# Optimization experiments

Hardware: AMD Instinct MI355X
Metric: run time of the kernel (lower is better)

The kernel has to match this reference:

```python
import jax, jax.numpy as jnp
import numpy as np

LAYERS, BLOCKS = 10, 4
NL = LAYERS * BLOCKS
RC, DC, SC, OUT_C = 32, 32, 256, 256
B, T = 4, 32768


def setup_inputs() -> dict:
    key = jax.random.key(0)
    ks = jax.random.split(key, 6)
    s = 0.1  # keep tanh out of saturation
    return {
        "x": jax.random.normal(ks[0], (B, 1, T), jnp.float32),
        "W_start": jax.random.normal(ks[1], (RC, 1), jnp.float32) * s,
        "b_start": jnp.zeros((RC,), jnp.float32),
        "Wd": jax.random.normal(ks[2], (NL, DC, RC, 2), jnp.float32) * s,  # torch conv1d weight (out,in,k)
        "bd": jnp.zeros((NL, DC), jnp.float32),
        "Wr": jax.random.normal(ks[3], (NL, RC, DC), jnp.float32) * s,     # 1x1 residual convs
        "br": jnp.zeros((NL, RC), jnp.float32),
        "Ws": jax.random.normal(ks[4], (NL, SC, DC), jnp.float32) * s,     # 1x1 skip convs
        "bs": jnp.zeros((NL, SC), jnp.float32),
        "Wf": jax.random.normal(ks[5], (OUT_C, SC), jnp.float32) * s,      # final 1x1 conv
        "bf": jnp.zeros((OUT_C,), jnp.float32),
    }


def _forward(x, W_start, b_start, Wd, bd, Wr, br, Ws, bs, Wf, bf):
    # start 1x1 conv: [B,1,T] -> [B,RC,T]
    h = jnp.einsum('oi,bit->bot', W_start, x) + b_start[:, None]
    skip = jnp.zeros((x.shape[0], SC, x.shape[2]), x.dtype)
    for i in range(NL):  # fixed small layer loop (40)
        d = 2 ** (i % LAYERS)
        # causal dilated conv, kernel=2: out[t] = W[...,0]@x[t-d] + W[...,1]@x[t]
        h_shift = jnp.pad(h, ((0, 0), (0, 0), (d, 0)))[:, :, : h.shape[2]]
        z = (jnp.einsum('oi,bit->bot', Wd[i, :, :, 1], h)
             + jnp.einsum('oi,bit->bot', Wd[i, :, :, 0], h_shift)
             + bd[i][:, None])
        z = jnp.tanh(z)
        r = jnp.einsum('oi,bit->bot', Wr[i], z) + br[i][:, None]
        h = h + r  # residual connection
        skip = skip + jnp.einsum('oi,bit->bot', Ws[i], h) + bs[i][:, None]
    out = jax.nn.relu(skip)
    return jnp.einsum('oi,bit->bot', Wf, out) + bf[:, None]


def reference(x, W_start, b_start, Wd, bd, Wr, br, Ws, bs, Wf, bf):
    return _forward(x, W_start, b_start, Wd, bd, Wr, br, Ws, bs, Wf, bf)
```

## Files before the change

### kernel.cpp

```cpp
#include <hip/hip_runtime.h>
#include <hip/hip_bf16.h>

#define T_LEN 32768
#define B_N   4
#define RC    32
#define DC    32
#define SC    256
#define OUTC  256
#define NL    40
#define KTOT  (NL * RC)
#define NBT   (B_N * T_LEN)
#define SLOTB ((size_t)NBT * 32 * 2)
#define BTW   64

typedef float f32x4 __attribute__((ext_vector_type(4)));
typedef short bf16x8 __attribute__((ext_vector_type(8)));
typedef __attribute__((address_space(3))) unsigned int lds_u32;
typedef __attribute__((address_space(3))) char lds_char;
typedef __attribute__((address_space(1))) unsigned int glb_u32;

__device__ __forceinline__ unsigned short f2bf_bits(float f) {
    __hip_bfloat16 b = __float2bfloat16(f);
    unsigned short u;
    __builtin_memcpy(&u, &b, 2);
    return u;
}
__device__ __forceinline__ unsigned pack2(float a, float b) {
    return (unsigned)f2bf_bits(a) | ((unsigned)f2bf_bits(b) << 16);
}
__device__ __forceinline__ float bflo(unsigned u) { return __uint_as_float((u & 0xFFFFu) << 16); }
__device__ __forceinline__ float bfhi(unsigned u) { return __uint_as_float(u & 0xFFFF0000u); }
__device__ __forceinline__ float ftanh(float x) {
    float e = __expf(2.f * x);
    return 1.f - 2.f / (e + 1.f);
}
__device__ __forceinline__ void wait_vmcnt(int n) {
    switch (n) {
        case 0: asm volatile("s_waitcnt vmcnt(0)" ::: "memory"); break;
        case 1: asm volatile("s_waitcnt vmcnt(1)" ::: "memory"); break;
        case 2: asm volatile("s_waitcnt vmcnt(2)" ::: "memory"); break;
        case 4: asm volatile("s_waitcnt vmcnt(4)" ::: "memory"); break;
        default: asm volatile("s_waitcnt vmcnt(8)" ::: "memory"); break;
    }
}

__global__ __launch_bounds__(256) void k_prep(const float* __restrict__ Ws,
                                              const float* __restrict__ Wf,
                                              const float* __restrict__ Wd,
                                              const float* __restrict__ Wr,
                                              const float* __restrict__ bs,
                                              unsigned short* __restrict__ Wsk2,
                                              unsigned short* __restrict__ Wfk,
                                              unsigned short* __restrict__ Wd1k,
                                              unsigned short* __restrict__ Wd0k,
                                              unsigned short* __restrict__ Wrk,
                                              float* __restrict__ bs_sum) {
    int g = blockIdx.x * 256 + threadIdx.x;
    if (g < SC * KTOT) {
        int i = g >> 13, r = g & 8191;
        int oc = r >> 5, c = r & 31;
        Wsk2[g] = f2bf_bits(Ws[(i * SC + oc) * RC + c]);
        return;
    }
    g -= SC * KTOT;
    if (g < OUTC * SC) { Wfk[g] = f2bf_bits(Wf[g]); return; }
    g -= OUTC * SC;
    if (g < NL * 1024) {
        int i = g >> 10, r = g & 1023;
        int o = r >> 5, c = r & 31;
        Wd1k[g] = f2bf_bits(Wd[((i * DC + o) * RC + c) * 2 + 1]);
        return;
    }
    g -= NL * 1024;
    if (g < NL * 1024) {
        int i = g >> 10, r = g & 1023;
        int o = r >> 5, c = r & 31;
        Wd0k[g] = f2bf_bits(Wd[((i * DC + o) * RC + c) * 2 + 0]);
        return;
    }
    g -= NL * 1024;
    if (g < NL * 1024) { Wrk[g] = f2bf_bits(Wr[g]); return; }
    g -= NL * 1024;
    if (g < SC) {
        float s = 0.f;
        for (int i = 0; i < NL; ++i) s += bs[i * SC + g];
        bs_sum[g] = s;
    }
}

__global__ __launch_bounds__(256) void k_start(const float* __restrict__ x,
                                               const float* __restrict__ Wst,
                                               const float* __restrict__ bst,
                                               unsigned short* __restrict__ h0) {
    int g = blockIdx.x * 256 + threadIdx.x;
    float xv = x[g];
    unsigned u[16];
#pragma unroll
    for (int q = 0; q < 16; ++q) {
        float a = Wst[2 * q] * xv + bst[2 * q];
        float b = Wst[2 * q + 1] * xv + bst[2 * q + 1];
        u[q] = pack2(a, b);
    }
    unsigned short* op = h0 + (size_t)g * 32;
#pragma unroll
    for (int q = 0; q < 4; ++q) *(uint4*)&op[q * 8] = *(uint4*)&u[q * 4];
}

__global__ __launch_bounds__(256, 4) void k_layer(const unsigned short* __restrict__ hprev,
                                                  unsigned short* __restrict__ hnext,
                                                  const unsigned short* __restrict__ Wd1k,
                                                  const unsigned short* __restrict__ Wd0k,
                                                  const unsigned short* __restrict__ Wrk,
                                                  const float* __restrict__ bd,
                                                  const float* __restrict__ br,
                                                  int d) {
    __shared__ unsigned short zbuf[4][32 * 40];
    int lane = threadIdx.x & 63;
    int wq = threadIdx.x >> 6;
    int lr = lane & 15, lg = lane >> 4;
    int btb = blockIdx.x * 128 + wq * 32;
    unsigned short* zp = &zbuf[wq][0];

    bf16x8 wd1[2], wd0[2], wr[2];
#pragma unroll
    for (int m = 0; m < 2; ++m) {
        int ao = (m * 16 + lr) * 32 + 8 * lg;
        wd1[m] = *(const bf16x8*)(Wd1k + ao);
        wd0[m] = *(const bf16x8*)(Wd0k + ao);
        wr[m]  = *(const bf16x8*)(Wrk + ao);
    }

    bf16x8 hc[2], hs[2];
    uint2 hcc[2][2];
#pragma unroll
    for (int n = 0; n < 2; ++n) {
        int bt = btb + n * 16 + lr;
        int t = bt & (T_LEN - 1);
        const unsigned short* hp = hprev + (size_t)bt * 32;
        hc[n] = *(const bf16x8*)(hp + 8 * lg);
        int bts = (t >= d) ? (bt - d) : bt;
        bf16x8 v = *(const bf16x8*)(hprev + (size_t)bts * 32 + 8 * lg);
        if (t < d) v = (bf16x8){0, 0, 0, 0, 0, 0, 0, 0};
        hs[n] = v;
#pragma unroll
        for (int m = 0; m < 2; ++m) hcc[n][m] = *(const uint2*)(hp + m * 16 + 4 * lg);
    }

    f32x4 zac[2][2];
#pragma unroll
    for (int m = 0; m < 2; ++m)
#pragma unroll
        for (int n = 0; n < 2; ++n) {
            f32x4 a = __builtin_amdgcn_mfma_f32_16x16x32_bf16(wd0[m], hs[n], (f32x4){0.f, 0.f, 0.f, 0.f}, 0, 0, 0);
            zac[m][n] = __builtin_amdgcn_mfma_f32_16x16x32_bf16(wd1[m], hc[n], a, 0, 0, 0);
        }

#pragma unroll
    for (int m = 0; m < 2; ++m) {
        float4 bdv = *(const float4*)(bd + m * 16 + 4 * lg);
#pragma unroll
        for (int n = 0; n < 2; ++n) {
            int rbt = n * 16 + lr;
            float z0 = ftanh(zac[m][n][0] + bdv.x);
            float z1 = ftanh(zac[m][n][1] + bdv.y);
            float z2 = ftanh(zac[m][n][2] + bdv.z);
            float z3 = ftanh(zac[m][n][3] + bdv.w);
            uint2 u;
            u.x = pack2(z0, z1);
            u.y = pack2(z2, z3);
            *(uint2*)(zp + rbt * 40 + m * 16 + 4 * lg) = u;
        }
    }

    f32x4 racc[2][2];
#pragma unroll
    for (int n = 0; n < 2; ++n) {
        int rbt = n * 16 + lr;
        bf16x8 zb = *(const bf16x8*)(zp + rbt * 40 + 8 * lg);
#pragma unroll
        for (int m = 0; m < 2; ++m)
            racc[m][n] = __builtin_amdgcn_mfma_f32_16x16x32_bf16(wr[m], zb, (f32x4){0.f, 0.f, 0.f, 0.f}, 0, 0, 0);
    }

#pragma unroll
    for (int m = 0; m < 2; ++m) {
        float4 brv = *(const float4*)(br + m * 16 + 4 * lg);
#pragma unroll
        for (int n = 0; n < 2; ++n) {
            int bt = btb + n * 16 + lr;
            float h0 = bflo(hcc[n][m].x) + racc[m][n][0] + brv.x;
            float h1 = bfhi(hcc[n][m].x) + racc[m][n][1] + brv.y;
            float h2 = bflo(hcc[n][m].y) + racc[m][n][2] + brv.z;
            float h3 = bfhi(hcc[n][m].y) + racc[m][n][3] + brv.w;
            uint2 u;
            u.x = pack2(h0, h1);
            u.y = pack2(h2, h3);
            *(uint2*)(hnext + (size_t)bt * 32 + m * 16 + 4 * lg) = u;
        }
    }
}

__global__ __launch_bounds__(512, 2) void k_skipfinal(const unsigned short* __restrict__ hist,
                                                      const unsigned short* __restrict__ Wsk2,
                                                      const unsigned short* __restrict__ Wfk,
                                                      const float* __restrict__ bs_sum,
                                                      const float* __restrict__ bfv,
                                                      float* __restrict__ outp) {
    __shared__ char smem[3 * 20480];
    const int tid = threadIdx.x;
    const int lane = tid & 63, wq = tid >> 6;
    const int lr = lane & 15, lg = lane >> 4;
    const int wm = wq & 3, wn = wq >> 2;
    const int bt0 = blockIdx.x * BTW;
    const char* histb = (const char*)hist;
    const char* Wsb = (const char*)Wsk2;
    lds_char* smem3 = (lds_char*)smem;

    int aoff[4], boff = 0;
    if (wq < 4) {
#pragma unroll
        for (int p = 0; p < 4; ++p) {
            int L = p * 4096 + tid * 16;
            int row = L >> 6, col = L & 63;
            aoff[p] = row * 64 + (col ^ ((row & 3) << 4));
        }
    } else {
        int L = (tid - 256) * 16;
        int row = L >> 6, col = L & 63;
        boff = (bt0 + row) * 64 + (col ^ ((row & 3) << 4));
    }

    auto stage = [&](int k) {
        char* base = smem + (k % 3) * 20480;
        if (wq < 4) {
#pragma unroll
            for (int p = 0; p < 4; ++p)
                __builtin_amdgcn_global_load_lds((const glb_u32*)(Wsb + (size_t)k * 16384 + aoff[p]),
                                                 (lds_u32*)(base + p * 4096 + tid * 16), 16, 0, 0);
        } else {
            __builtin_amdgcn_global_load_lds((const glb_u32*)(histb + (size_t)k * SLOTB + boff),
                                             (lds_u32*)(base + 16384 + (tid - 256) * 16), 16, 0, 0);
        }
    };

    f32x4 acc[4][2];
#pragma unroll
    for (int m = 0; m < 4; ++m)
#pragma unroll
        for (int n = 0; n < 2; ++n) acc[m][n] = (f32x4){0.f, 0.f, 0.f, 0.f};

    const int cswz = (lg * 16) ^ ((lr & 3) << 4);
    const int arow = wm * 64 + lr;
    const int brow = wn * 32 + lr;

    stage(0);
    stage(1);

#pragma unroll
    for (int i = 0; i < NL; ++i) {
        if (i + 2 < NL) stage(i + 2);
        if (wq < 4) wait_vmcnt(i <= 37 ? 8 : (i == 38 ? 4 : 0));
        else        wait_vmcnt(i <= 37 ? 2 : (i == 38 ? 1 : 0));
        __builtin_amdgcn_s_barrier();

        lds_char* Ab = smem3 + (i % 3) * 20480;
        lds_char* Bb = Ab + 16384;
        bf16x8 af0, af1, af2, af3, bf0, bf1;
        asm volatile("ds_read_b128 %0, %1" : "=v"(af0) : "v"(Ab + (arow + 0) * 64 + cswz));
        asm volatile("ds_read_b128 %0, %1" : "=v"(af1) : "v"(Ab + (arow + 16) * 64 + cswz));
        asm volatile("ds_read_b128 %0, %1" : "=v"(af2) : "v"(Ab + (arow + 32) * 64 + cswz));
        asm volatile("ds_read_b128 %0, %1" : "=v"(af3) : "v"(Ab + (arow + 48) * 64 + cswz));
        asm volatile("ds_read_b128 %0, %1" : "=v"(bf0) : "v"(Bb + (brow + 0) * 64 + cswz));
        asm volatile("ds_read_b128 %0, %1" : "=v"(bf1) : "v"(Bb + (brow + 16) * 64 + cswz));
        asm volatile("s_waitcnt lgkmcnt(0)" ::: "memory");
        __builtin_amdgcn_sched_barrier(0);

        acc[0][0] = __builtin_amdgcn_mfma_f32_16x16x32_bf16(af0, bf0, acc[0][0], 0, 0, 0);
        acc[1][0] = __builtin_amdgcn_mfma_f32_16x16x32_bf16(af1, bf0, acc[1][0], 0, 0, 0);
        acc[2][0] = __builtin_amdgcn_mfma_f32_16x16x32_bf16(af2, bf0, acc[2][0], 0, 0, 0);
        acc[3][0] = __builtin_amdgcn_mfma_f32_16x16x32_bf16(af3, bf0, acc[3][0], 0, 0, 0);
        acc[0][1] = __builtin_amdgcn_mfma_f32_16x16x32_bf16(af0, bf1, acc[0][1], 0, 0, 0);
        acc[1][1] = __builtin_amdgcn_mfma_f32_16x16x32_bf16(af1, bf1, acc[1][1], 0, 0, 0);
        acc[2][1] = __builtin_amdgcn_mfma_f32_16x16x32_bf16(af2, bf1, acc[2][1], 0, 0, 0);
        acc[3][1] = __builtin_amdgcn_mfma_f32_16x16x32_bf16(af3, bf1, acc[3][1], 0, 0, 0);
        __builtin_amdgcn_s_barrier();
    }
    __syncthreads();

    char* skb = smem;
#pragma unroll
    for (int m = 0; m < 4; ++m) {
        int oc0 = wm * 64 + m * 16 + lg * 4;
        float c0 = bs_sum[oc0], c1 = bs_sum[oc0 + 1], c2 = bs_sum[oc0 + 2], c3 = bs_sum[oc0 + 3];
#pragma unroll
        for (int n = 0; n < 2; ++n) {
            int bt = wn * 32 + n * 16 + lr;
            f32x4 v = acc[m][n];
            uint2 u;
            u.x = pack2(fmaxf(v[0] + c0, 0.f), fmaxf(v[1] + c1, 0.f));
            u.y = pack2(fmaxf(v[2] + c2, 0.f), fmaxf(v[3] + c3, 0.f));
            int L = bt * 512 + oc0 * 2;
            *(uint2*)(skb + (L ^ ((bt & 7) << 4))) = u;
        }
    }
    __syncthreads();

    f32x4 acc2[4][2];
#pragma unroll
    for (int m = 0; m < 4; ++m)
#pragma unroll
        for (int n = 0; n < 2; ++n) acc2[m][n] = (f32x4){0.f, 0.f, 0.f, 0.f};

    const unsigned short* Fb = Wfk + (size_t)(wm * 64 + lr) * SC + 8 * lg;

#pragma unroll
    for (int kk = 0; kk < SC / 32; ++kk) {
        bf16x8 fa[4];
#pragma unroll
        for (int m = 0; m < 4; ++m) fa[m] = *(const bf16x8*)(Fb + (size_t)m * 16 * SC + kk * 32);
        bf16x8 sbv[2];
#pragma unroll
        for (int n = 0; n < 2; ++n) {
            int bt = wn * 32 + n * 16 + lr;
            int L = bt * 512 + kk * 64 + lg * 16;
            sbv[n] = *(const bf16x8*)(skb + (L ^ ((bt & 7) << 4)));
        }
#pragma unroll
        for (int m = 0; m < 4; ++m)
#pragma unroll
            for (int n = 0; n < 2; ++n)
                acc2[m][n] = __builtin_amdgcn_mfma_f32_16x16x32_bf16(fa[m], sbv[n], acc2[m][n], 0, 0, 0);
    }

    int b2 = bt0 >> 15;
    int t0 = bt0 & (T_LEN - 1);
#pragma unroll
    for (int m = 0; m < 4; ++m) {
        int o0 = wm * 64 + m * 16 + lg * 4;
        float q0 = bfv[o0], q1 = bfv[o0 + 1], q2 = bfv[o0 + 2], q3 = bfv[o0 + 3];
#pragma unroll
        for (int n = 0; n < 2; ++n) {
            int t = t0 + wn * 32 + n * 16 + lr;
            f32x4 v = acc2[m][n];
            outp[((size_t)(b2 * OUTC + o0 + 0) << 15) + t] = v[0] + q0;
            outp[((size_t)(b2 * OUTC + o0 + 1) << 15) + t] = v[1] + q1;
            outp[((size_t)(b2 * OUTC + o0 + 2) << 15) + t] = v[2] + q2;
            outp[((size_t)(b2 * OUTC + o0 + 3) << 15) + t] = v[3] + q3;
        }
    }
}

extern "C" void kernel_launch(void* const* d_in, const int* in_sizes, int n_in,
                              void* d_out, int out_size, void* d_ws, size_t ws_size,
                              hipStream_t stream) {
    const float* x       = (const float*)d_in[0];
    const float* W_start = (const float*)d_in[1];
    const float* b_start = (const float*)d_in[2];
    const float* Wd      = (const float*)d_in[3];
    const float* bd      = (const float*)d_in[4];
    const float* Wr      = (const float*)d_in[5];
    const float* br      = (const float*)d_in[6];
    const float* Ws      = (const float*)d_in[7];
    const float* bs      = (const float*)d_in[8];
    const float* Wf      = (const float*)d_in[9];
    const float* bfv     = (const float*)d_in[10];

    char* wsb = (char*)d_ws;
    unsigned short* Wsk2 = (unsigned short*)(wsb);
    unsigned short* Wfk  = (unsigned short*)(wsb + 655360);
    unsigned short* Wd1k = (unsigned short*)(wsb + 786432);
    unsigned short* Wd0k = (unsigned short*)(wsb + 868352);
    unsigned short* Wrk  = (unsigned short*)(wsb + 950272);
    float*          bs_sum = (float*)(wsb + 1032192);
    char* S1 = wsb + (1 << 20);
    char* X  = S1 + 40 * SLOTB;

    auto slotptr = [&](int i) -> unsigned short* {
        return (unsigned short*)(i == 0 ? X : S1 + (size_t)(i - 1) * SLOTB);
    };

    k_prep<<<(SC * KTOT + OUTC * SC + 3 * NL * 1024 + SC + 255) / 256, 256, 0, stream>>>(
        Ws, Wf, Wd, Wr, bs, Wsk2, Wfk, Wd1k, Wd0k, Wrk, bs_sum);
    k_start<<<NBT / 256, 256, 0, stream>>>(x, W_start, b_start, slotptr(0));

    for (int i = 0; i < NL; ++i) {
        int d = 1 << (i % 10);
        k_layer<<<NBT / 128, 256, 0, stream>>>(slotptr(i), slotptr(i + 1),
                                               Wd1k + i * 1024, Wd0k + i * 1024, Wrk + i * 1024,
                                               bd + i * DC, br + i * RC, d);
    }

    k_skipfinal<<<NBT / BTW, 512, 0, stream>>>((unsigned short*)S1, Wsk2, Wfk, bs_sum, bfv, (float*)d_out);
}
```

Measured before the change: 489.5 us.

## Double skip-GEMM column tile and switch to a two-slot LDS ring

The skip/final kernel now covers 128 time steps per block instead of 64. Each wave computes a 64x64 tile, so every staged slice of skip weights is reused across twice as many columns. Staging moves from a three-slot ring, with waves split between weight and history loads, to a two-slot ring in which every thread loads both. The row swizzle is adjusted to the new tile shapes. The launch-bounds occupancy hint goes from 2 to 4 blocks while accumulators double, which risks register spills. The 64 KB LDS per block may also cap real occupancy below that hint.

```diff
diff --git a/kernel.cpp b/kernel.cpp
--- a/kernel.cpp
+++ b/kernel.cpp
@@ -11,7 +11,8 @@
 #define KTOT  (NL * RC)
 #define NBT   (B_N * T_LEN)
 #define SLOTB ((size_t)NBT * 32 * 2)
-#define BTW   64
+#define BTW   128
+#define RING  24576
 
 typedef float f32x4 __attribute__((ext_vector_type(4)));
 typedef short bf16x8 __attribute__((ext_vector_type(8)));
@@ -34,15 +35,7 @@
     float e = __expf(2.f * x);
     return 1.f - 2.f / (e + 1.f);
 }
-__device__ __forceinline__ void wait_vmcnt(int n) {
-    switch (n) {
-        case 0: asm volatile("s_waitcnt vmcnt(0)" ::: "memory"); break;
-        case 1: asm volatile("s_waitcnt vmcnt(1)" ::: "memory"); break;
-        case 2: asm volatile("s_waitcnt vmcnt(2)" ::: "memory"); break;
-        case 4: asm volatile("s_waitcnt vmcnt(4)" ::: "memory"); break;
-        default: asm volatile("s_waitcnt vmcnt(8)" ::: "memory"); break;
-    }
-}
+__device__ __forceinline__ int swz(int L) { return L ^ ((((L >> 7) & 3)) << 4); }
 
 __global__ __launch_bounds__(256) void k_prep(const float* __restrict__ Ws,
                                               const float* __restrict__ Wf,
@@ -200,13 +193,13 @@
     }
 }
 
-__global__ __launch_bounds__(512, 2) void k_skipfinal(const unsigned short* __restrict__ hist,
+__global__ __launch_bounds__(512, 4) void k_skipfinal(const unsigned short* __restrict__ hist,
                                                       const unsigned short* __restrict__ Wsk2,
                                                       const unsigned short* __restrict__ Wfk,
                                                       const float* __restrict__ bs_sum,
                                                       const float* __restrict__ bfv,
                                                       float* __restrict__ outp) {
-    __shared__ char smem[3 * 20480];
+    __shared__ char smem[65536];
     const int tid = threadIdx.x;
     const int lane = tid & 63, wq = tid >> 6;
     const int lr = lane & 15, lg = lane >> 4;
@@ -216,73 +209,75 @@
     const char* Wsb = (const char*)Wsk2;
     lds_char* smem3 = (lds_char*)smem;
 
-    int aoff[4], boff = 0;
-    if (wq < 4) {
-#pragma unroll
-        for (int p = 0; p < 4; ++p) {
-            int L = p * 4096 + tid * 16;
-            int row = L >> 6, col = L & 63;
-            aoff[p] = row * 64 + (col ^ ((row & 3) << 4));
-        }
-    } else {
-        int L = (tid - 256) * 16;
-        int row = L >> 6, col = L & 63;
-        boff = (bt0 + row) * 64 + (col ^ ((row & 3) << 4));
+    int asrc[2], bsrc;
+#pragma unroll
+    for (int p = 0; p < 2; ++p) asrc[p] = swz(p * 8192 + tid * 16);
+    bsrc = (size_t)0;
+    {
+        int D = tid * 16;
+        bsrc = bt0 * 64 + swz(D);
     }
 
     auto stage = [&](int k) {
-        char* base = smem + (k % 3) * 20480;
-        if (wq < 4) {
-#pragma unroll
-            for (int p = 0; p < 4; ++p)
-                __builtin_amdgcn_global_load_lds((const glb_u32*)(Wsb + (size_t)k * 16384 + aoff[p]),
-                                                 (lds_u32*)(base + p * 4096 + tid * 16), 16, 0, 0);
-        } else {
-            __builtin_amdgcn_global_load_lds((const glb_u32*)(histb + (size_t)k * SLOTB + boff),
-                                             (lds_u32*)(base + 16384 + (tid - 256) * 16), 16, 0, 0);
-        }
+        char* base = smem + (k & 1) * RING;
+#pragma unroll
+        for (int p = 0; p < 2; ++p)
+            __builtin_amdgcn_global_load_lds((const glb_u32*)(Wsb + (size_t)k * 16384 + asrc[p]),
+                                             (lds_u32*)(base + p * 8192 + tid * 16), 16, 0, 0);
+        __builtin_amdgcn_global_load_lds((const glb_u32*)(histb + (size_t)k * SLOTB + bsrc),
+                                         (lds_u32*)(base + 16384 + tid * 16), 16, 0, 0);
     };
 
-    f32x4 acc[4][2];
+    f32x4 acc[4][4];
 #pragma unroll
     for (int m = 0; m < 4; ++m)
 #pragma unroll
-        for (int n = 0; n < 2; ++n) acc[m][n] = (f32x4){0.f, 0.f, 0.f, 0.f};
-
-    const int cswz = (lg * 16) ^ ((lr & 3) << 4);
+        for (int n = 0; n < 4; ++n) acc[m][n] = (f32x4){0.f, 0.f, 0.f, 0.f};
+
+    const int cswz = (lg * 16) ^ (((lr >> 1) & 3) << 4);
     const int arow = wm * 64 + lr;
-    const int brow = wn * 32 + lr;
+    const int brow = wn * 64 + lr;
 
     stage(0);
     stage(1);
 
 #pragma unroll
     for (int i = 0; i < NL; ++i) {
-        if (i + 2 < NL) stage(i + 2);
-        if (wq < 4) wait_vmcnt(i <= 37 ? 8 : (i == 38 ? 4 : 0));
-        else        wait_vmcnt(i <= 37 ? 2 : (i == 38 ? 1 : 0));
+        if (i >= 1 && i + 1 < NL) stage(i + 1);
+        if (i + 1 < NL) asm volatile("s_waitcnt vmcnt(3)" ::: "memory");
+        else            asm volatile("s_waitcnt vmcnt(0)" ::: "memory");
         __builtin_amdgcn_s_barrier();
 
-        lds_char* Ab = smem3 + (i % 3) * 20480;
+        lds_char* Ab = smem3 + (i & 1) * RING;
         lds_char* Bb = Ab + 16384;
-        bf16x8 af0, af1, af2, af3, bf0, bf1;
+        bf16x8 af0, af1, af2, af3, bb0, bb1, bb2, bb3;
         asm volatile("ds_read_b128 %0, %1" : "=v"(af0) : "v"(Ab + (arow + 0) * 64 + cswz));
         asm volatile("ds_read_b128 %0, %1" : "=v"(af1) : "v"(Ab + (arow + 16) * 64 + cswz));
         asm volatile("ds_read_b128 %0, %1" : "=v"(af2) : "v"(Ab + (arow + 32) * 64 + cswz));
         asm volatile("ds_read_b128 %0, %1" : "=v"(af3) : "v"(Ab + (arow + 48) * 64 + cswz));
-        asm volatile("ds_read_b128 %0, %1" : "=v"(bf0) : "v"(Bb + (brow + 0) * 64 + cswz));
-        asm volatile("ds_read_b128 %0, %1" : "=v"(bf1) : "v"(Bb + (brow + 16) * 64 + cswz));
+        asm volatile("ds_read_b128 %0, %1" : "=v"(bb0) : "v"(Bb + (brow + 0) * 64 + cswz));
+        asm volatile("ds_read_b128 %0, %1" : "=v"(bb1) : "v"(Bb + (brow + 16) * 64 + cswz));
+        asm volatile("ds_read_b128 %0, %1" : "=v"(bb2) : "v"(Bb + (brow + 32) * 64 + cswz));
+        asm volatile("ds_read_b128 %0, %1" : "=v"(bb3) : "v"(Bb + (brow + 48) * 64 + cswz));
         asm volatile("s_waitcnt lgkmcnt(0)" ::: "memory");
         __builtin_amdgcn_sched_barrier(0);
 
-        acc[0][0] = __builtin_amdgcn_mfma_f32_16x16x32_bf16(af0, bf0, acc[0][0], 0, 0, 0);
-        acc[1][0] = __builtin_amdgcn_mfma_f32_16x16x32_bf16(af1, bf0, acc[1][0], 0, 0, 0);
-        acc[2][0] = __builtin_amdgcn_mfma_f32_16x16x32_bf16(af2, bf0, acc[2][0], 0, 0, 0);
-        acc[3][0] = __builtin_amdgcn_mfma_f32_16x16x32_bf16(af3, bf0, acc[3][0], 0, 0, 0);
-        acc[0][1] = __builtin_amdgcn_mfma_f32_16x16x32_bf16(af0, bf1, acc[0][1], 0, 0, 0);
-        acc[1][1] = __builtin_amdgcn_mfma_f32_16x16x32_bf16(af1, bf1, acc[1][1], 0, 0, 0);
-        acc[2][1] = __builtin_amdgcn_mfma_f32_16x16x32_bf16(af2, bf1, acc[2][1], 0, 0, 0);
-        acc[3][1] = __builtin_amdgcn_mfma_f32_16x16x32_bf16(af3, bf1, acc[3][1], 0, 0, 0);
+        acc[0][0] = __builtin_amdgcn_mfma_f32_16x16x32_bf16(af0, bb0, acc[0][0], 0, 0, 0);
+        acc[1][0] = __builtin_amdgcn_mfma_f32_16x16x32_bf16(af1, bb0, acc[1][0], 0, 0, 0);
+        acc[2][0] = __builtin_amdgcn_mfma_f32_16x16x32_bf16(af2, bb0, acc[2][0], 0, 0, 0);
+        acc[3][0] = __builtin_amdgcn_mfma_f32_16x16x32_bf16(af3, bb0, acc[3][0], 0, 0, 0);
+        acc[0][1] = __builtin_amdgcn_mfma_f32_16x16x32_bf16(af0, bb1, acc[0][1], 0, 0, 0);
+        acc[1][1] = __builtin_amdgcn_mfma_f32_16x16x32_bf16(af1, bb1, acc[1][1], 0, 0, 0);
+        acc[2][1] = __builtin_amdgcn_mfma_f32_16x16x32_bf16(af2, bb1, acc[2][1], 0, 0, 0);
+        acc[3][1] = __builtin_amdgcn_mfma_f32_16x16x32_bf16(af3, bb1, acc[3][1], 0, 0, 0);
+        acc[0][2] = __builtin_amdgcn_mfma_f32_16x16x32_bf16(af0, bb2, acc[0][2], 0, 0, 0);
+        acc[1][2] = __builtin_amdgcn_mfma_f32_16x16x32_bf16(af1, bb2, acc[1][2], 0, 0, 0);
+        acc[2][2] = __builtin_amdgcn_mfma_f32_16x16x32_bf16(af2, bb2, acc[2][2], 0, 0, 0);
+        acc[3][2] = __builtin_amdgcn_mfma_f32_16x16x32_bf16(af3, bb2, acc[3][2], 0, 0, 0);
+        acc[0][3] = __builtin_amdgcn_mfma_f32_16x16x32_bf16(af0, bb3, acc[0][3], 0, 0, 0);
+        acc[1][3] = __builtin_amdgcn_mfma_f32_16x16x32_bf16(af1, bb3, acc[1][3], 0, 0, 0);
+        acc[2][3] = __builtin_amdgcn_mfma_f32_16x16x32_bf16(af2, bb3, acc[2][3], 0, 0, 0);
+        acc[3][3] = __builtin_amdgcn_mfma_f32_16x16x32_bf16(af3, bb3, acc[3][3], 0, 0, 0);
         __builtin_amdgcn_s_barrier();
     }
     __syncthreads();
@@ -293,8 +288,8 @@
         int oc0 = wm * 64 + m * 16 + lg * 4;
         float c0 = bs_sum[oc0], c1 = bs_sum[oc0 + 1], c2 = bs_sum[oc0 + 2], c3 = bs_sum[oc0 + 3];
 #pragma unroll
-        for (int n = 0; n < 2; ++n) {
-            int bt = wn * 32 + n * 16 + lr;
+        for (int n = 0; n < 4; ++n) {
+            int bt = wn * 64 + n * 16 + lr;
             f32x4 v = acc[m][n];
             uint2 u;
             u.x = pack2(fmaxf(v[0] + c0, 0.f), fmaxf(v[1] + c1, 0.f));
@@ -305,11 +300,11 @@
     }
     __syncthreads();
 
-    f32x4 acc2[4][2];
+    f32x4 acc2[4][4];
 #pragma unroll
     for (int m = 0; m < 4; ++m)
 #pragma unroll
-        for (int n = 0; n < 2; ++n) acc2[m][n] = (f32x4){0.f, 0.f, 0.f, 0.f};
+        for (int n = 0; n < 4; ++n) acc2[m][n] = (f32x4){0.f, 0.f, 0.f, 0.f};
 
     const unsigned short* Fb = Wfk + (size_t)(wm * 64 + lr) * SC + 8 * lg;
 
@@ -318,17 +313,17 @@
         bf16x8 fa[4];
 #pragma unroll
         for (int m = 0; m < 4; ++m) fa[m] = *(const bf16x8*)(Fb + (size_t)m * 16 * SC + kk * 32);
-        bf16x8 sbv[2];
-#pragma unroll
-        for (int n = 0; n < 2; ++n) {
-            int bt = wn * 32 + n * 16 + lr;
+        bf16x8 sbv[4];
+#pragma unroll
+        for (int n = 0; n < 4; ++n) {
+            int bt = wn * 64 + n * 16 + lr;
             int L = bt * 512 + kk * 64 + lg * 16;
             sbv[n] = *(const bf16x8*)(skb + (L ^ ((bt & 7) << 4)));
         }
 #pragma unroll
         for (int m = 0; m < 4; ++m)
 #pragma unroll
-            for (int n = 0; n < 2; ++n)
+            for (int n = 0; n < 4; ++n)
                 acc2[m][n] = __builtin_amdgcn_mfma_f32_16x16x32_bf16(fa[m], sbv[n], acc2[m][n], 0, 0, 0);
     }
 
@@ -339,8 +334,8 @@
         int o0 = wm * 64 + m * 16 + lg * 4;
         float q0 = bfv[o0], q1 = bfv[o0 + 1], q2 = bfv[o0 + 2], q3 = bfv[o0 + 3];
 #pragma unroll
-        for (int n = 0; n < 2; ++n) {
-            int t = t0 + wn * 32 + n * 16 + lr;
+        for (int n = 0; n < 4; ++n) {
+            int t = t0 + wn * 64 + n * 16 + lr;
             f32x4 v = acc2[m][n];
             outp[((size_t)(b2 * OUTC + o0 + 0) << 15) + t] = v[0] + q0;
             outp[((size_t)(b2 * OUTC + o0 + 1) << 15) + t] = v[1] + q1;
```

Result: faster. 448.4 us (-8.4%).
